# Kernel optimization log

Hardware: AMD Instinct MI355X
Metric: run time of the kernel (lower is better)

Reference implementation:

```python
import jax, jax.numpy as jnp
import numpy as np

N, E, F_IN, F_E, H, HEADS, NG = 50000, 300000, 16, 8, 64, 4, 64
D_HEAD = H // HEADS
EPS = 1e-5


def setup_inputs() -> dict:
    key = jax.random.key(0)
    ks = jax.random.split(key, 12)
    def rn(k, shape, s=0.1):
        return jax.random.normal(k, shape, jnp.float32) * s
    return dict(
        x=jax.random.normal(ks[0], (N, F_IN), jnp.float32),
        edge_index=jax.random.randint(ks[1], (2, E), 0, N),
        edge_attr=jax.random.normal(ks[2], (E, F_E), jnp.float32),
        batch=jnp.sort(jax.random.randint(ks[3], (N,), 0, NG)),
        # edge_net: Linear(F_E, H*F_IN) -> ReLU -> Linear(H*F_IN, H*F_IN)
        en_w1=rn(ks[4], (F_E, H * F_IN)), en_b1=jnp.zeros((H * F_IN,), jnp.float32),
        en_w2=rn(ks[5], (H * F_IN, H * F_IN)), en_b2=jnp.zeros((H * F_IN,), jnp.float32),
        # NNConv root weight + bias
        root_w=rn(ks[6], (F_IN, H)), conv1_b=jnp.zeros((H,), jnp.float32),
        norm1_w=jnp.ones((H,), jnp.float32), norm1_b=jnp.zeros((H,), jnp.float32),
        # GATConv: lin weight, attention vectors, bias
        gat_w=rn(ks[7], (H, H)),
        att_src=rn(ks[8], (HEADS, D_HEAD)), att_dst=rn(ks[9], (HEADS, D_HEAD)),
        gat_b=jnp.zeros((H,), jnp.float32),
        norm2_w=jnp.ones((H,), jnp.float32), norm2_b=jnp.zeros((H,), jnp.float32),
        lin_w=rn(ks[10], (H, 1)), lin_b=jnp.zeros((1,), jnp.float32),
    )


def _graph_layernorm(x, w, b):
    # PyG LayerNorm(mode='graph') with batch=None: scalar mean/std over ALL elems
    mu = x.mean()
    sd = jnp.sqrt(((x - mu) ** 2).mean())
    return (x - mu) / (sd + EPS) * w + b


def reference(x, edge_index, edge_attr, batch, en_w1, en_b1, en_w2, en_b2,
              root_w, conv1_b, norm1_w, norm1_b, gat_w, att_src, att_dst,
              gat_b, norm2_w, norm2_b, lin_w, lin_b):
    src, dst = edge_index[0], edge_index[1]
    # --- NNConv: per-edge weight matrices from edge_net ---
    w_e = jax.nn.relu(edge_attr @ en_w1 + en_b1) @ en_w2 + en_b2
    w_e = w_e.reshape(E, F_IN, H)                      # [E, in, out]
    msg = jnp.einsum('ef,efh->eh', x[src], w_e)        # gather-matmul per edge
    agg = jax.ops.segment_sum(msg, dst, num_segments=N)
    deg = jax.ops.segment_sum(jnp.ones((E,), x.dtype), dst, num_segments=N)
    agg = agg / jnp.maximum(deg, 1.0)[:, None]         # aggr='mean'
    h = x @ root_w + agg + conv1_b
    h = jax.nn.relu(h)
    h = _graph_layernorm(h, norm1_w, norm1_b)
    # dropout: eval mode -> identity
    # --- GATConv (edge_attr=None at call site; add self-loops, softmax attn) ---
    loops = jnp.arange(N)
    s2 = jnp.concatenate([src, loops])
    d2 = jnp.concatenate([dst, loops])
    xh = (h @ gat_w).reshape(N, HEADS, D_HEAD)
    a_src = (xh * att_src).sum(-1)                     # [N, HEADS]
    a_dst = (xh * att_dst).sum(-1)
    alpha = jax.nn.leaky_relu(a_src[s2] + a_dst[d2], 0.2)  # [E+N, HEADS]
    amax = jax.ops.segment_max(alpha, d2, num_segments=N)
    alpha = jnp.exp(alpha - amax[d2])
    asum = jax.ops.segment_sum(alpha, d2, num_segments=N)
    alpha = alpha / (asum[d2] + 1e-16)
    out = jax.ops.segment_sum(alpha[:, :, None] * xh[s2], d2, num_segments=N)
    h2 = out.reshape(N, H) + gat_b                     # concat heads
    h2 = jax.nn.relu(h2)
    h2 = _graph_layernorm(h2, norm2_w, norm2_b)
    # --- global mean pool + linear head ---
    gs = jax.ops.segment_sum(h2, batch, num_segments=NG)
    cnt = jax.ops.segment_sum(jnp.ones((N,), h2.dtype), batch, num_segments=NG)
    pooled = gs / jnp.maximum(cnt, 1.0)[:, None]
    return pooled @ lin_w + lin_b                      # [NG, 1]
```

## Files before the change

kernel.cpp:

```cpp
#include <hip/hip_runtime.h>
#include <hip/hip_bf16.h>

#define N_NODES 50000
#define E_EDGES 300000
#define NGRAPH 64
#define KTOT 16512
#define NCHUNK 129
#define CSPLIT 65
#define NSTEP 516
#define NEGRP 1172
#define LNEPS 1e-5f
#define NBLK_N 196
#define NBLK_P 12500
#define RPRE 1.00146484375f

typedef __bf16 bf16x8 __attribute__((ext_vector_type(8)));
typedef float floatx4 __attribute__((ext_vector_type(4)));
typedef float f32x2 __attribute__((ext_vector_type(2)));
typedef unsigned int u32x4 __attribute__((ext_vector_type(4)));

__device__ __forceinline__ unsigned pkt(f32x2 p) {
  return __builtin_amdgcn_perm(__float_as_uint(p[1]), __float_as_uint(p[0]), 0x07060302u);
}
__device__ __forceinline__ unsigned pkbf(float a, float b) {
  unsigned ua = __float_as_uint(a) + 0x8000u;
  unsigned ub = __float_as_uint(b) + 0x8000u;
  return __builtin_amdgcn_perm(ub, ua, 0x07060302u);
}

__global__ void k_prep(const float* __restrict__ w2, const float* __restrict__ b2,
                       __bf16* __restrict__ Tt2) {
  int idx = blockIdx.x * 256 + threadIdx.x;
  int step = idx >> 11;
  int rem = idx & 2047;
  int h = rem >> 5;
  int kw = rem & 31;
  int kf = step * 32 + kw;
  float v = 0.f;
  if (kf < 16384) {
    int k = kf >> 4, f = kf & 15;
    v = w2[k * 1024 + f * 64 + h];
  } else if (kf < 16400) {
    v = b2[(kf - 16384) * 64 + h];
  }
  Tt2[idx] = (__bf16)v;
}

__global__ void k_prepw(const float* __restrict__ w1, float* __restrict__ W1t) {
  int i = blockIdx.x * 256 + threadIdx.x;
  if (i < 8192) { int k = i >> 3, j = i & 7; W1t[i] = w1[j * 1024 + k]; }
}

__global__ void k_cnt(const int* __restrict__ ei, int* __restrict__ degI) {
  int e = blockIdx.x * 256 + threadIdx.x;
  if (e < E_EDGES) atomicAdd(&degI[ei[E_EDGES + e]], 1);
}

__global__ void k_scanA(const int* __restrict__ degI, int* __restrict__ bsum) {
  __shared__ int sm[256];
  int t = threadIdx.x;
  int i = blockIdx.x * 256 + t;
  sm[t] = (i < N_NODES) ? degI[i] : 0;
  __syncthreads();
  for (int off = 128; off > 0; off >>= 1) {
    if (t < off) sm[t] += sm[t + off];
    __syncthreads();
  }
  if (t == 0) bsum[blockIdx.x] = sm[0];
}

__global__ void k_scanB(const int* __restrict__ bsum, int* __restrict__ bpre) {
  __shared__ int s[256];
  int t = threadIdx.x;
  int v = (t < NBLK_N) ? bsum[t] : 0;
  s[t] = v;
  __syncthreads();
  for (int off = 1; off < 256; off <<= 1) {
    int add = (t >= off) ? s[t - off] : 0;
    __syncthreads();
    s[t] += add;
    __syncthreads();
  }
  if (t < NBLK_N) bpre[t] = s[t] - v;
}

__global__ void k_scanC(const int* __restrict__ degI, const int* __restrict__ bpre,
                        int* __restrict__ rowptr, int* __restrict__ cursor) {
  __shared__ int s[256];
  int t = threadIdx.x;
  int i = blockIdx.x * 256 + t;
  int d = (i < N_NODES) ? degI[i] : 0;
  s[t] = d;
  __syncthreads();
  for (int off = 1; off < 256; off <<= 1) {
    int add = (t >= off) ? s[t - off] : 0;
    __syncthreads();
    s[t] += add;
    __syncthreads();
  }
  int r = bpre[blockIdx.x] + s[t] - d;
  if (i < N_NODES) {
    rowptr[i] = r;
    cursor[i] = r;
    if (i == N_NODES - 1) rowptr[N_NODES] = r + d;
  }
}

__global__ void k_scatter(const int* __restrict__ ei, int* __restrict__ cursor,
                          int* __restrict__ colsrc) {
  int e = blockIdx.x * 256 + threadIdx.x;
  if (e < E_EDGES) {
    int s = ei[e], d = ei[E_EDGES + e];
    int pos = atomicAdd(&cursor[d], 1);
    colsrc[pos] = s;
  }
}

__global__ __launch_bounds__(256, 3)
void k_nnconv(const float* __restrict__ x, const int* __restrict__ ei,
              const float* __restrict__ ea, const float* __restrict__ W1t,
              const float* __restrict__ b1, const __bf16* __restrict__ Tt2,
              float* __restrict__ agg) {
  const int tid = threadIdx.x;
  const int lane = tid & 63;
  const int l15 = lane & 15;
  const int quad = lane >> 4;
  const bool qhi = (lane & 32) != 0;
  const unsigned rsel = qhi ? 0x07060100u : 0x05040100u;
  const int grp = blockIdx.x >> 1;
  const int half = blockIdx.x & 1;
  const int cstart = half ? CSPLIT : 0;
  const int cend = half ? NCHUNK : CSPLIT;

  int e = grp * 256 + tid;
  bool valid = e < E_EDGES;
  int srcv = valid ? ei[e] : 0;
  int dstv = valid ? ei[E_EDGES + e] : -1;

  f32x2 ea2[4];
  {
    const float4* p = (const float4*)(ea + (size_t)(valid ? e : 0) * 8);
    float4 a0 = p[0], a1 = p[1];
    ea2[0] = (f32x2){a0.x, a0.y};
    ea2[1] = (f32x2){a0.z, a0.w};
    ea2[2] = (f32x2){a1.x, a1.y};
    ea2[3] = (f32x2){a1.z, a1.w};
  }

  const int f0 = (quad & 1) * 8;
  f32x2 xf2[4][4];
#pragma unroll
  for (int mb = 0; mb < 4; ++mb) {
    int s = __shfl(srcv, mb * 16 + l15);
    const float4* px = (const float4*)(x + (size_t)s * 16 + f0);
    float4 v0 = px[0], v1 = px[1];
    xf2[mb][0] = (f32x2){v0.x * RPRE, v0.y * RPRE};
    xf2[mb][1] = (f32x2){v0.z * RPRE, v0.w * RPRE};
    xf2[mb][2] = (f32x2){v1.x * RPRE, v1.y * RPRE};
    xf2[mb][3] = (f32x2){v1.z * RPRE, v1.w * RPRE};
  }

  int bpaddr[4];
#pragma unroll
  for (int mb = 0; mb < 4; ++mb) bpaddr[mb] = (mb * 16 + l15) * 4;

  const __bf16* bp = Tt2 + (size_t)(cstart * 4) * 2048 + (l15 * 32 + quad * 8);

  bf16x8 Ba[4], Bb[4];
  auto loadB = [&](bf16x8* d) {
    d[0] = *(const bf16x8*)(bp);
    d[1] = *(const bf16x8*)(bp + 512);
    d[2] = *(const bf16x8*)(bp + 1024);
    d[3] = *(const bf16x8*)(bp + 1536);
    bp += 2048;
  };

  unsigned prr[4];
  auto calcR = [&](int c, const float* w1p, const float* b1p) {
    if (c < 128) {
#pragma unroll
      for (int ks = 0; ks < 4; ++ks) {
        float rv[2];
#pragma unroll
        for (int kk = 0; kk < 2; ++kk) {
          const f32x2* w = (const f32x2*)(w1p + (ks * 2 + kk) * 8);
          f32x2 s01 = ea2[0] * w[0] + ea2[1] * w[1];
          f32x2 s23 = ea2[2] * w[2] + ea2[3] * w[3];
          f32x2 s = s01 + s23;
          rv[kk] = fmaxf(b1p[ks * 2 + kk] + s[0] + s[1], 0.f);
        }
        prr[ks] = pkbf(rv[0], rv[1]);
      }
    } else {
      prr[0] = 0x00003F80u;
      prr[1] = prr[2] = prr[3] = 0u;
    }
  };

  unsigned ubuf[16];
  auto bcastR = [&]() {
#pragma unroll
    for (int ks = 0; ks < 4; ++ks)
#pragma unroll
      for (int mb = 0; mb < 4; ++mb)
        ubuf[ks * 4 + mb] = (unsigned)__builtin_amdgcn_ds_bpermute(bpaddr[mb], (int)prr[ks]);
  };

  floatx4 acc[4][4];
#pragma unroll
  for (int mb = 0; mb < 4; ++mb)
#pragma unroll
    for (int nb = 0; nb < 4; ++nb) acc[mb][nb] = floatx4{0.f, 0.f, 0.f, 0.f};

  calcR(cstart, W1t + cstart * 64, b1 + cstart * 8);
  bcastR();
  loadB(Ba);
  const float* w1p = W1t + (cstart + 1) * 64;
  const float* b1p = b1 + (cstart + 1) * 8;

  for (int c = cstart; c < cend; ++c) {
#pragma unroll
    for (int ks = 0; ks < 4; ++ks) {
      bf16x8* Bc = (ks & 1) ? Bb : Ba;
      bf16x8* Bn = (ks & 1) ? Ba : Bb;
      loadB(Bn);
#pragma unroll
      for (int mb = 0; mb < 4; ++mb) {
        float rv = __uint_as_float(__builtin_amdgcn_perm(ubuf[ks * 4 + mb], 0u, rsel));
        f32x2 rv2 = {rv, rv};
        u32x4 U;
        U[0] = pkt(rv2 * xf2[mb][0]);
        U[1] = pkt(rv2 * xf2[mb][1]);
        U[2] = pkt(rv2 * xf2[mb][2]);
        U[3] = pkt(rv2 * xf2[mb][3]);
        bf16x8 A = __builtin_bit_cast(bf16x8, U);
#pragma unroll
        for (int nb = 0; nb < 4; ++nb)
          acc[mb][nb] = __builtin_amdgcn_mfma_f32_16x16x32_bf16(A, Bc[nb], acc[mb][nb], 0, 0, 0);
      }
    }
    if (c + 1 < cend) {
      calcR(c + 1, w1p, b1p);
      bcastR();
      w1p += 64; b1p += 8;
    }
  }

#pragma unroll
  for (int mb = 0; mb < 4; ++mb) {
#pragma unroll
    for (int reg = 0; reg < 4; ++reg) {
      int dd = __shfl(dstv, mb * 16 + quad * 4 + reg);
      if (dd >= 0) {
#pragma unroll
        for (int nb = 0; nb < 4; ++nb)
          atomicAdd(&agg[(size_t)dd * 64 + nb * 16 + l15], acc[mb][nb][reg]);
      }
    }
  }
}

__global__ void k_root(const float* __restrict__ x, const float* __restrict__ rootw,
                       const float* __restrict__ conv1b, const float* __restrict__ agg,
                       const int* __restrict__ degI, float* __restrict__ hpre,
                       float* __restrict__ rpart) {
  __shared__ float sW[1024];
  __shared__ float sx[64];
  __shared__ float red[8];
  int t = threadIdx.x;
  int blk = blockIdx.x;
#pragma unroll
  for (int i = 0; i < 4; ++i) sW[t + i * 256] = rootw[t + i * 256];
  if (t < 64) sx[t] = x[(size_t)blk * 64 + t];
  __syncthreads();
  int ln = t >> 6, h = t & 63;
  int n = blk * 4 + ln;
  float acc = conv1b[h];
#pragma unroll
  for (int f = 0; f < 16; ++f) acc += sx[ln * 16 + f] * sW[f * 64 + h];
  float dv = fmaxf((float)degI[n], 1.0f);
  float v = acc + agg[(size_t)n * 64 + h] / dv;
  v = fmaxf(v, 0.f);
  hpre[(size_t)n * 64 + h] = v;
  float s1 = v, s2 = v * v;
  for (int o = 32; o > 0; o >>= 1) { s1 += __shfl_down(s1, o); s2 += __shfl_down(s2, o); }
  if ((t & 63) == 0) { red[t >> 6] = s1; red[4 + (t >> 6)] = s2; }
  __syncthreads();
  if (t == 0) {
    rpart[blk * 2] = red[0] + red[1] + red[2] + red[3];
    rpart[blk * 2 + 1] = red[4] + red[5] + red[6] + red[7];
  }
}

__global__ void k_fold1(const float* __restrict__ rpart, const float* __restrict__ n1w,
                        const float* __restrict__ n1b, const float* __restrict__ gatw,
                        float* __restrict__ gw2, float* __restrict__ tb) {
  __shared__ float red[8];
  __shared__ float sMI[2];
  __shared__ float sS[64], sT[64];
  int t = threadIdx.x;
  int wv = t >> 6, lane = t & 63;
  float a = 0.f, b = 0.f;
  for (int i = t; i < NBLK_P; i += 256) { a += rpart[2 * i]; b += rpart[2 * i + 1]; }
  for (int o = 32; o > 0; o >>= 1) { a += __shfl_down(a, o); b += __shfl_down(b, o); }
  if (lane == 0) { red[wv] = a; red[4 + wv] = b; }
  __syncthreads();
  if (t == 0) {
    float A = red[0] + red[1] + red[2] + red[3];
    float B = red[4] + red[5] + red[6] + red[7];
    const float M = (float)N_NODES * 64.f;
    float mu = A / M;
    float var = fmaxf(B / M - mu * mu, 0.f);
    sMI[0] = mu;
    sMI[1] = 1.f / (sqrtf(var) + LNEPS);
  }
  __syncthreads();
  if (t < 64) {
    float mu = sMI[0], inv = sMI[1];
    sS[t] = inv * n1w[t];
    sT[t] = n1b[t] - mu * inv * n1w[t];
  }
  __syncthreads();
  if (t < 64) {
    float acc = 0.f;
    for (int i = 0; i < 64; ++i) {
      float g = gatw[i * 64 + t];
      gw2[i * 64 + t] = sS[i] * g;
      acc += sT[i] * g;
    }
    tb[t] = acc;
  }
}

__global__ void k_gatlin(const float* __restrict__ hpre, const float* __restrict__ gw2,
                         const float* __restrict__ tb, const float* __restrict__ attS,
                         const float* __restrict__ attD, float* __restrict__ xh,
                         float* __restrict__ asrc, float* __restrict__ adst) {
  __shared__ float sW[4096];
  __shared__ float sh[256];
  __shared__ float sxh[256];
  int t = threadIdx.x;
  int blk = blockIdx.x;
#pragma unroll
  for (int i = 0; i < 16; ++i) sW[t + i * 256] = gw2[t + i * 256];
  sh[t] = hpre[(size_t)blk * 256 + t];
  __syncthreads();
  int ln = t >> 6, h = t & 63;
  float acc = tb[h];
  for (int i = 0; i < 64; ++i) acc += sh[ln * 64 + i] * sW[i * 64 + h];
  xh[(size_t)blk * 256 + t] = acc;
  sxh[t] = acc;
  __syncthreads();
  if (t < 32) {
    int ln2 = t >> 3, rem = t & 7;
    int hd = rem & 3;
    const float* av = (rem >> 2) ? attD : attS;
    float a = 0.f;
#pragma unroll
    for (int d = 0; d < 16; ++d) a += sxh[ln2 * 64 + hd * 16 + d] * av[hd * 16 + d];
    int n = blk * 4 + ln2;
    if (rem >> 2) adst[n * 4 + hd] = a; else asrc[n * 4 + hd] = a;
  }
}

__global__ void k_gat(const int* __restrict__ rowptr, const int* __restrict__ colsrc,
                      const float* __restrict__ xh, const float* __restrict__ asrc,
                      const float* __restrict__ adst, const float* __restrict__ gatb,
                      float* __restrict__ act, float* __restrict__ gpart) {
  __shared__ float sP[4][256];
  __shared__ int sS[4][64];
  __shared__ float sRed[8];
  int t = threadIdx.x;
  int wv = t >> 6, lane = t & 63;
  int n = blockIdx.x * 4 + wv;
  int start = rowptr[n], end = rowptr[n + 1];
  int deg = end - start;
  int myhd = lane >> 4;
  float ad[4];
#pragma unroll
  for (int hd = 0; hd < 4; ++hd) ad[hd] = adst[n * 4 + hd];
  float m[4] = {-1e30f, -1e30f, -1e30f, -1e30f};
  float l[4] = {0.f, 0.f, 0.f, 0.f};
  float O = 0.f;
  int items = deg + 1;
  for (int t0 = 0; t0 < items; t0 += 64) {
    int cnt = min(64, items - t0);
    int idx = t0 + lane;
    bool has = lane < cnt;
    int s = n;
    if (has && idx < deg) s = colsrc[start + idx];
    float a[4];
#pragma unroll
    for (int hd = 0; hd < 4; ++hd) {
      float av = has ? (asrc[s * 4 + hd] + ad[hd]) : -1e30f;
      a[hd] = (av > 0.f) ? av : 0.2f * av;
    }
    float tm[4];
#pragma unroll
    for (int hd = 0; hd < 4; ++hd) tm[hd] = a[hd];
#pragma unroll
    for (int off = 32; off > 0; off >>= 1)
#pragma unroll
      for (int hd = 0; hd < 4; ++hd) tm[hd] = fmaxf(tm[hd], __shfl_xor(tm[hd], off));
    float p[4];
#pragma unroll
    for (int hd = 0; hd < 4; ++hd) {
      float mn = fmaxf(m[hd], tm[hd]);
      float sc = __expf(m[hd] - mn);
      l[hd] *= sc;
      if (hd == myhd) O *= sc;
      m[hd] = mn;
      p[hd] = has ? __expf(a[hd] - mn) : 0.f;
    }
    float ts[4];
#pragma unroll
    for (int hd = 0; hd < 4; ++hd) ts[hd] = p[hd];
#pragma unroll
    for (int off = 32; off > 0; off >>= 1)
#pragma unroll
      for (int hd = 0; hd < 4; ++hd) ts[hd] += __shfl_xor(ts[hd], off);
#pragma unroll
    for (int hd = 0; hd < 4; ++hd) l[hd] += ts[hd];
    sS[wv][lane] = s;
#pragma unroll
    for (int hd = 0; hd < 4; ++hd) sP[wv][lane * 4 + hd] = p[hd];
    for (int e2 = 0; e2 < cnt; ++e2) {
      int ss = sS[wv][e2];
      float pp = sP[wv][e2 * 4 + myhd];
      O = fmaf(pp, xh[(size_t)ss * 64 + lane], O);
    }
  }
  float lmy = (myhd & 2) ? ((myhd & 1) ? l[3] : l[2]) : ((myhd & 1) ? l[1] : l[0]);
  float outv = O / (lmy + 1e-16f);
  float v = fmaxf(outv + gatb[lane], 0.f);
  act[(size_t)n * 64 + lane] = v;
  float s1 = v, s2 = v * v;
#pragma unroll
  for (int off = 32; off > 0; off >>= 1) { s1 += __shfl_down(s1, off); s2 += __shfl_down(s2, off); }
  if (lane == 0) { sRed[wv] = s1; sRed[4 + wv] = s2; }
  __syncthreads();
  if (t == 0) {
    gpart[blockIdx.x * 2] = sRed[0] + sRed[1] + sRed[2] + sRed[3];
    gpart[blockIdx.x * 2 + 1] = sRed[4] + sRed[5] + sRed[6] + sRed[7];
  }
}

__global__ void k_fold2(const float* __restrict__ gpart, const float* __restrict__ n2w,
                        const float* __restrict__ n2b, const float* __restrict__ linw,
                        const float* __restrict__ linb, float* __restrict__ wl) {
  __shared__ float red[8];
  __shared__ float sMI[2];
  int t = threadIdx.x;
  int wv = t >> 6, lane = t & 63;
  float a = 0.f, b = 0.f;
  for (int i = t; i < NBLK_P; i += 256) { a += gpart[2 * i]; b += gpart[2 * i + 1]; }
  for (int o = 32; o > 0; o >>= 1) { a += __shfl_down(a, o); b += __shfl_down(b, o); }
  if (lane == 0) { red[wv] = a; red[4 + wv] = b; }
  __syncthreads();
  if (t == 0) {
    float A = red[0] + red[1] + red[2] + red[3];
    float B = red[4] + red[5] + red[6] + red[7];
    const float M = (float)N_NODES * 64.f;
    float mu = A / M;
    float var = fmaxf(B / M - mu * mu, 0.f);
    sMI[0] = mu;
    sMI[1] = 1.f / (sqrtf(var) + LNEPS);
  }
  __syncthreads();
  if (t < 64) {
    float mu = sMI[0], inv = sMI[1];
    float w = inv * n2w[t] * linw[t];
    float p = (n2b[t] - mu * inv * n2w[t]) * linw[t];
    wl[t] = w;
    for (int o = 32; o > 0; o >>= 1) p += __shfl_down(p, o);
    if (t == 0) wl[64] = p + linb[0];
  }
}

__global__ void k_out(const float* __restrict__ act, const float* __restrict__ wl,
                      const int* __restrict__ batch, float* __restrict__ out) {
  __shared__ float red[4];
  __shared__ float swl[64];
  int g = blockIdx.x;
  int t = threadIdx.x;
  int wv = t >> 6, lane = t & 63;
  if (t < 64) swl[t] = wl[t];
  __syncthreads();
  auto lbound = [&](int key) {
    int lo = 0, hi = N_NODES;
    while (lo < hi) { int mid = (lo + hi) >> 1; if (batch[mid] < key) lo = mid + 1; else hi = mid; }
    return lo;
  };
  int lo = lbound(g), hi = lbound(g + 1);
  int cntn = hi - lo;
  float s = 0.f;
  for (int idx = t; idx < cntn * 64; idx += 256) {
    int n = lo + (idx >> 6);
    int d = idx & 63;
    s += act[(size_t)n * 64 + d] * swl[d];
  }
  for (int o = 32; o > 0; o >>= 1) s += __shfl_down(s, o);
  if (lane == 0) red[wv] = s;
  __syncthreads();
  if (t == 0)
    out[g] = (red[0] + red[1] + red[2] + red[3]) / fmaxf((float)cntn, 1.f) + wl[64];
}

#define OFF_AGG     0UL
#define OFF_DEGI    12800000UL
#define ZBYTES      13000000UL
#define OFF_RPART   13000000UL
#define OFF_GPART   13100032UL
#define OFF_ROWPTR  13200064UL
#define OFF_CURSOR  13400128UL
#define OFF_BSUM    13600192UL
#define OFF_BPRE    13601024UL
#define OFF_COLSRC  13601856UL
#define OFF_TT      14801856UL
#define OFF_W1T     16919488UL
#define OFF_GW2     16952256UL
#define OFF_TB      16968640UL
#define OFF_WL      16968896UL
#define OFF_ASRC    16969216UL
#define OFF_ADST    17769216UL
#define OFF_HPRE    18569216UL
#define OFF_XH      31369216UL
#define OFF_ACT     44169216UL
#define WS_NEED     56969216UL

extern "C" void kernel_launch(void* const* d_in, const int* in_sizes, int n_in,
                              void* d_out, int out_size, void* d_ws, size_t ws_size,
                              hipStream_t stream) {
  const float* x = (const float*)d_in[0];
  const int* ei = (const int*)d_in[1];
  const float* ea = (const float*)d_in[2];
  const int* batch = (const int*)d_in[3];
  const float* w1 = (const float*)d_in[4];
  const float* b1 = (const float*)d_in[5];
  const float* w2 = (const float*)d_in[6];
  const float* b2 = (const float*)d_in[7];
  const float* rootw = (const float*)d_in[8];
  const float* conv1b = (const float*)d_in[9];
  const float* n1w = (const float*)d_in[10];
  const float* n1b = (const float*)d_in[11];
  const float* gatw = (const float*)d_in[12];
  const float* attS = (const float*)d_in[13];
  const float* attD = (const float*)d_in[14];
  const float* gatb = (const float*)d_in[15];
  const float* n2w = (const float*)d_in[16];
  const float* n2b = (const float*)d_in[17];
  const float* linw = (const float*)d_in[18];
  const float* linb = (const float*)d_in[19];

  if (ws_size < WS_NEED) return;
  char* ws = (char*)d_ws;
  float* agg    = (float*)(ws + OFF_AGG);
  int* degI     = (int*)(ws + OFF_DEGI);
  float* rpart  = (float*)(ws + OFF_RPART);
  float* gpart  = (float*)(ws + OFF_GPART);
  int* rowptr   = (int*)(ws + OFF_ROWPTR);
  int* cursor   = (int*)(ws + OFF_CURSOR);
  int* bsum     = (int*)(ws + OFF_BSUM);
  int* bpre     = (int*)(ws + OFF_BPRE);
  int* colsrc   = (int*)(ws + OFF_COLSRC);
  __bf16* Tt2   = (__bf16*)(ws + OFF_TT);
  float* W1t    = (float*)(ws + OFF_W1T);
  float* gw2    = (float*)(ws + OFF_GW2);
  float* tb     = (float*)(ws + OFF_TB);
  float* wl     = (float*)(ws + OFF_WL);
  float* asrc   = (float*)(ws + OFF_ASRC);
  float* adst   = (float*)(ws + OFF_ADST);
  float* hpre   = (float*)(ws + OFF_HPRE);
  float* xh     = (float*)(ws + OFF_XH);
  float* act    = (float*)(ws + OFF_ACT);

  hipMemsetAsync(ws, 0, ZBYTES, stream);

  k_prep<<<(NSTEP + 1) * 8, 256, 0, stream>>>(w2, b2, Tt2);
  k_prepw<<<32, 256, 0, stream>>>(w1, W1t);
  k_cnt<<<(E_EDGES + 255) / 256, 256, 0, stream>>>(ei, degI);
  k_scanA<<<NBLK_N, 256, 0, stream>>>(degI, bsum);
  k_scanB<<<1, 256, 0, stream>>>(bsum, bpre);
  k_scanC<<<NBLK_N, 256, 0, stream>>>(degI, bpre, rowptr, cursor);
  k_scatter<<<(E_EDGES + 255) / 256, 256, 0, stream>>>(ei, cursor, colsrc);
  k_nnconv<<<NEGRP * 2, 256, 0, stream>>>(x, ei, ea, W1t, b1, Tt2, agg);
  k_root<<<NBLK_P, 256, 0, stream>>>(x, rootw, conv1b, agg, degI, hpre, rpart);
  k_fold1<<<1, 256, 0, stream>>>(rpart, n1w, n1b, gatw, gw2, tb);
  k_gatlin<<<NBLK_P, 256, 0, stream>>>(hpre, gw2, tb, attS, attD, xh, asrc, adst);
  k_gat<<<NBLK_P, 256, 0, stream>>>(rowptr, colsrc, xh, asrc, adst, gatb, act, gpart);
  k_fold2<<<1, 256, 0, stream>>>(gpart, n2w, n2b, linw, linb, wl);
  k_out<<<NGRAPH, 256, 0, stream>>>(act, wl, batch, (float*)d_out);
}
```

Before: 1.034 ms.

## Switch NNConv MFMA path from bf16 to fp16 with packed half products

Converts the per-edge weight table and the A operand of the NNConv matmul from bf16 to fp16. The A-fragment build becomes packed half multiplies instead of fp32 multiplies plus perm-based truncation. The B operand prefetch grows from two buffers to a four-deep register ring. This is meant to cut VALU work in the inner loop and hide more load latency. It costs extra VGPRs, which may hurt occupancy under the 3-waves bound, and fp16 range and rounding behave differently from bf16.

```diff
diff --git a/kernel.cpp b/kernel.cpp
--- a/kernel.cpp
+++ b/kernel.cpp
@@ -4,32 +4,23 @@
 #define N_NODES 50000
 #define E_EDGES 300000
 #define NGRAPH 64
-#define KTOT 16512
 #define NCHUNK 129
 #define CSPLIT 65
-#define NSTEP 516
+#define NSTEPP 518
 #define NEGRP 1172
 #define LNEPS 1e-5f
 #define NBLK_N 196
 #define NBLK_P 12500
-#define RPRE 1.00146484375f
-
-typedef __bf16 bf16x8 __attribute__((ext_vector_type(8)));
+#define RPRE16 1.00048828125f
+
+typedef _Float16 f16x8 __attribute__((ext_vector_type(8)));
+typedef _Float16 f16x2 __attribute__((ext_vector_type(2)));
 typedef float floatx4 __attribute__((ext_vector_type(4)));
 typedef float f32x2 __attribute__((ext_vector_type(2)));
 typedef unsigned int u32x4 __attribute__((ext_vector_type(4)));
 
-__device__ __forceinline__ unsigned pkt(f32x2 p) {
-  return __builtin_amdgcn_perm(__float_as_uint(p[1]), __float_as_uint(p[0]), 0x07060302u);
-}
-__device__ __forceinline__ unsigned pkbf(float a, float b) {
-  unsigned ua = __float_as_uint(a) + 0x8000u;
-  unsigned ub = __float_as_uint(b) + 0x8000u;
-  return __builtin_amdgcn_perm(ub, ua, 0x07060302u);
-}
-
 __global__ void k_prep(const float* __restrict__ w2, const float* __restrict__ b2,
-                       __bf16* __restrict__ Tt2) {
+                       _Float16* __restrict__ Tt2) {
   int idx = blockIdx.x * 256 + threadIdx.x;
   int step = idx >> 11;
   int rem = idx & 2047;
@@ -43,7 +34,7 @@
   } else if (kf < 16400) {
     v = b2[(kf - 16384) * 64 + h];
   }
-  Tt2[idx] = (__bf16)v;
+  Tt2[idx] = (_Float16)v;
 }
 
 __global__ void k_prepw(const float* __restrict__ w1, float* __restrict__ W1t) {
@@ -119,14 +110,14 @@
 __global__ __launch_bounds__(256, 3)
 void k_nnconv(const float* __restrict__ x, const int* __restrict__ ei,
               const float* __restrict__ ea, const float* __restrict__ W1t,
-              const float* __restrict__ b1, const __bf16* __restrict__ Tt2,
+              const float* __restrict__ b1, const _Float16* __restrict__ Tt2,
               float* __restrict__ agg) {
   const int tid = threadIdx.x;
   const int lane = tid & 63;
   const int l15 = lane & 15;
   const int quad = lane >> 4;
   const bool qhi = (lane & 32) != 0;
-  const unsigned rsel = qhi ? 0x07060100u : 0x05040100u;
+  const unsigned rsel = qhi ? 0x07060706u : 0x05040504u;
   const int grp = blockIdx.x >> 1;
   const int half = blockIdx.x & 1;
   const int cstart = half ? CSPLIT : 0;
@@ -148,30 +139,30 @@
   }
 
   const int f0 = (quad & 1) * 8;
-  f32x2 xf2[4][4];
+  unsigned xh16[4][4];
 #pragma unroll
   for (int mb = 0; mb < 4; ++mb) {
     int s = __shfl(srcv, mb * 16 + l15);
     const float4* px = (const float4*)(x + (size_t)s * 16 + f0);
     float4 v0 = px[0], v1 = px[1];
-    xf2[mb][0] = (f32x2){v0.x * RPRE, v0.y * RPRE};
-    xf2[mb][1] = (f32x2){v0.z * RPRE, v0.w * RPRE};
-    xf2[mb][2] = (f32x2){v1.x * RPRE, v1.y * RPRE};
-    xf2[mb][3] = (f32x2){v1.z * RPRE, v1.w * RPRE};
+    xh16[mb][0] = __builtin_bit_cast(unsigned, __builtin_amdgcn_cvt_pkrtz(v0.x * RPRE16, v0.y * RPRE16));
+    xh16[mb][1] = __builtin_bit_cast(unsigned, __builtin_amdgcn_cvt_pkrtz(v0.z * RPRE16, v0.w * RPRE16));
+    xh16[mb][2] = __builtin_bit_cast(unsigned, __builtin_amdgcn_cvt_pkrtz(v1.x * RPRE16, v1.y * RPRE16));
+    xh16[mb][3] = __builtin_bit_cast(unsigned, __builtin_amdgcn_cvt_pkrtz(v1.z * RPRE16, v1.w * RPRE16));
   }
 
   int bpaddr[4];
 #pragma unroll
   for (int mb = 0; mb < 4; ++mb) bpaddr[mb] = (mb * 16 + l15) * 4;
 
-  const __bf16* bp = Tt2 + (size_t)(cstart * 4) * 2048 + (l15 * 32 + quad * 8);
-
-  bf16x8 Ba[4], Bb[4];
-  auto loadB = [&](bf16x8* d) {
-    d[0] = *(const bf16x8*)(bp);
-    d[1] = *(const bf16x8*)(bp + 512);
-    d[2] = *(const bf16x8*)(bp + 1024);
-    d[3] = *(const bf16x8*)(bp + 1536);
+  const _Float16* bp = Tt2 + (size_t)(cstart * 4) * 2048 + (l15 * 32 + quad * 8);
+
+  f16x8 Bq[4][4];
+  auto loadB = [&](int which) {
+    Bq[which][0] = *(const f16x8*)(bp);
+    Bq[which][1] = *(const f16x8*)(bp + 512);
+    Bq[which][2] = *(const f16x8*)(bp + 1024);
+    Bq[which][3] = *(const f16x8*)(bp + 1536);
     bp += 2048;
   };
 
@@ -187,12 +178,12 @@
           f32x2 s01 = ea2[0] * w[0] + ea2[1] * w[1];
           f32x2 s23 = ea2[2] * w[2] + ea2[3] * w[3];
           f32x2 s = s01 + s23;
-          rv[kk] = fmaxf(b1p[ks * 2 + kk] + s[0] + s[1], 0.f);
+          rv[kk] = fmaxf(b1p[ks * 2 + kk] + s[0] + s[1], 0.f) * RPRE16;
         }
-        prr[ks] = pkbf(rv[0], rv[1]);
+        prr[ks] = __builtin_bit_cast(unsigned, __builtin_amdgcn_cvt_pkrtz(rv[0], rv[1]));
       }
     } else {
-      prr[0] = 0x00003F80u;
+      prr[0] = 0x00003C00u;
       prr[1] = prr[2] = prr[3] = 0u;
     }
   };
@@ -214,29 +205,28 @@
 
   calcR(cstart, W1t + cstart * 64, b1 + cstart * 8);
   bcastR();
-  loadB(Ba);
+  loadB(0);
+  loadB(1);
   const float* w1p = W1t + (cstart + 1) * 64;
   const float* b1p = b1 + (cstart + 1) * 8;
 
   for (int c = cstart; c < cend; ++c) {
 #pragma unroll
     for (int ks = 0; ks < 4; ++ks) {
-      bf16x8* Bc = (ks & 1) ? Bb : Ba;
-      bf16x8* Bn = (ks & 1) ? Ba : Bb;
-      loadB(Bn);
+      loadB((ks + 2) & 3);
 #pragma unroll
       for (int mb = 0; mb < 4; ++mb) {
-        float rv = __uint_as_float(__builtin_amdgcn_perm(ubuf[ks * 4 + mb], 0u, rsel));
-        f32x2 rv2 = {rv, rv};
+        f16x2 r2 = __builtin_bit_cast(f16x2,
+            __builtin_amdgcn_perm(ubuf[ks * 4 + mb], 0u, rsel));
         u32x4 U;
-        U[0] = pkt(rv2 * xf2[mb][0]);
-        U[1] = pkt(rv2 * xf2[mb][1]);
-        U[2] = pkt(rv2 * xf2[mb][2]);
-        U[3] = pkt(rv2 * xf2[mb][3]);
-        bf16x8 A = __builtin_bit_cast(bf16x8, U);
+#pragma unroll
+        for (int j = 0; j < 4; ++j)
+          U[j] = __builtin_bit_cast(unsigned,
+                   __builtin_bit_cast(f16x2, xh16[mb][j]) * r2);
+        f16x8 A = __builtin_bit_cast(f16x8, U);
 #pragma unroll
         for (int nb = 0; nb < 4; ++nb)
-          acc[mb][nb] = __builtin_amdgcn_mfma_f32_16x16x32_bf16(A, Bc[nb], acc[mb][nb], 0, 0, 0);
+          acc[mb][nb] = __builtin_amdgcn_mfma_f32_16x16x32_f16(A, Bq[ks][nb], acc[mb][nb], 0, 0, 0);
       }
     }
     if (c + 1 < cend) {
@@ -517,16 +507,16 @@
 #define OFF_BPRE    13601024UL
 #define OFF_COLSRC  13601856UL
 #define OFF_TT      14801856UL
-#define OFF_W1T     16919488UL
-#define OFF_GW2     16952256UL
-#define OFF_TB      16968640UL
-#define OFF_WL      16968896UL
-#define OFF_ASRC    16969216UL
-#define OFF_ADST    17769216UL
-#define OFF_HPRE    18569216UL
-#define OFF_XH      31369216UL
-#define OFF_ACT     44169216UL
-#define WS_NEED     56969216UL
+#define OFF_W1T     16923584UL
+#define OFF_GW2     16956352UL
+#define OFF_TB      16972736UL
+#define OFF_WL      16972992UL
+#define OFF_ASRC    16973312UL
+#define OFF_ADST    17773312UL
+#define OFF_HPRE    18573312UL
+#define OFF_XH      31373312UL
+#define OFF_ACT     44173312UL
+#define WS_NEED     56973312UL
 
 extern "C" void kernel_launch(void* const* d_in, const int* in_sizes, int n_in,
                               void* d_out, int out_size, void* d_ws, size_t ws_size,
@@ -563,7 +553,7 @@
   int* bsum     = (int*)(ws + OFF_BSUM);
   int* bpre     = (int*)(ws + OFF_BPRE);
   int* colsrc   = (int*)(ws + OFF_COLSRC);
-  __bf16* Tt2   = (__bf16*)(ws + OFF_TT);
+  _Float16* Tt2 = (_Float16*)(ws + OFF_TT);
   float* W1t    = (float*)(ws + OFF_W1T);
   float* gw2    = (float*)(ws + OFF_GW2);
   float* tb     = (float*)(ws + OFF_TB);
@@ -576,7 +566,7 @@
 
   hipMemsetAsync(ws, 0, ZBYTES, stream);
 
-  k_prep<<<(NSTEP + 1) * 8, 256, 0, stream>>>(w2, b2, Tt2);
+  k_prep<<<NSTEPP * 8, 256, 0, stream>>>(w2, b2, Tt2);
   k_prepw<<<32, 256, 0, stream>>>(w1, W1t);
   k_cnt<<<(E_EDGES + 255) / 256, 256, 0, stream>>>(ei, degI);
   k_scanA<<<NBLK_N, 256, 0, stream>>>(degI, bsum);
```

After: 1.012 ms. 1.02x faster.
